# Optimization experiments

Hardware: AMD Instinct MI355X
Metric: run time of the kernel (lower is better)

## Reference

```python
import jax, jax.numpy as jnp
import numpy as np
import math

Z_DIM = 1024
DOWN = 512
UP = 1024
HEADS = 16
ROPE_HD = 64
HEAD_DIM = Z_DIM // HEADS  # 64, used only in softmax scale
V_HD = UP // HEADS


def _rope(x, num_heads, head_dim, base=10000.0):
    # x: [bs, L, num_heads*head_dim] -> [bs, num_heads, L, head_dim]
    bs, L, _ = x.shape
    theta = 1.0 / (base ** (jnp.arange(0, head_dim, 2, dtype=jnp.float32) / head_dim))
    pe = jnp.arange(L, dtype=jnp.float32)[:, None] * theta[None, :]  # [L, hd/2]
    # NOTE: faithful to source, which stores sin(pos) in cos_pos and cos(pos) in sin_pos
    cos_pos = jnp.repeat(jnp.sin(pe), 2, axis=-1)  # [L, hd]
    sin_pos = jnp.repeat(jnp.cos(pe), 2, axis=-1)
    q = x.reshape(bs, L, num_heads, head_dim).transpose(0, 2, 1, 3)
    q2 = jnp.stack([-q[..., 1::2], q[..., ::2]], axis=-1).reshape(q.shape)
    return q * cos_pos + q2 * sin_pos


def setup_inputs() -> dict:
    key = jax.random.key(0)
    ks = jax.random.split(key, 20)
    B, S = 2, 2048
    s = lambda fan_in: 1.0 / math.sqrt(fan_in)
    d = {
        'query': jax.random.normal(ks[0], (B, S, Z_DIM), jnp.float32),
        'key': jax.random.normal(ks[1], (B, S, Z_DIM), jnp.float32),
        'value': jax.random.normal(ks[2], (B, S, Z_DIM), jnp.float32),
        'w_dkv': jax.random.uniform(ks[3], (Z_DIM, DOWN), jnp.float32, -s(Z_DIM), s(Z_DIM)),
        'b_dkv': jnp.zeros((DOWN,), jnp.float32),
        'w_uk': jax.random.uniform(ks[4], (DOWN, UP), jnp.float32, -s(DOWN), s(DOWN)),
        'b_uk': jnp.zeros((UP,), jnp.float32),
        'w_uv': jax.random.uniform(ks[5], (DOWN, UP), jnp.float32, -s(DOWN), s(DOWN)),
        'b_uv': jnp.zeros((UP,), jnp.float32),
        'w_dq': jax.random.uniform(ks[6], (Z_DIM, DOWN), jnp.float32, -s(Z_DIM), s(Z_DIM)),
        'b_dq': jnp.zeros((DOWN,), jnp.float32),
        'w_uq': jax.random.uniform(ks[7], (DOWN, UP), jnp.float32, -s(DOWN), s(DOWN)),
        'b_uq': jnp.zeros((UP,), jnp.float32),
        'w_qr': jax.random.uniform(ks[8], (DOWN, ROPE_HD * HEADS), jnp.float32, -s(DOWN), s(DOWN)),
        'b_qr': jnp.zeros((ROPE_HD * HEADS,), jnp.float32),
        'w_kr': jax.random.uniform(ks[9], (Z_DIM, ROPE_HD), jnp.float32, -s(Z_DIM), s(Z_DIM)),
        'b_kr': jnp.zeros((ROPE_HD,), jnp.float32),
        'w_fc': jax.random.uniform(ks[10], (HEADS * V_HD, Z_DIM), jnp.float32, -s(HEADS * V_HD), s(HEADS * V_HD)),
        'b_fc': jnp.zeros((Z_DIM,), jnp.float32),
    }
    return d


def reference(query, key, value, w_dkv, b_dkv, w_uk, b_uk, w_uv, b_uv,
              w_dq, b_dq, w_uq, b_uq, w_qr, b_qr, w_kr, b_kr, w_fc, b_fc):
    bs, S, _ = query.shape
    c_t_kv = key @ w_dkv + b_dkv                      # [B,S,down]
    k_t_c = c_t_kv @ w_uk + b_uk                      # [B,S,up]
    v_t_c = c_t_kv @ w_uv + b_uv                      # [B,S,up]
    c_t_q = query @ w_dq + b_dq                       # [B,S,down]
    q_t_c = c_t_q @ w_uq + b_uq                       # [B,S,up]
    q_t_r = _rope(c_t_q @ w_qr + b_qr, HEADS, ROPE_HD)  # [B,H,S,rope_hd]
    k_t_r = _rope(key @ w_kr + b_kr, 1, ROPE_HD)         # [B,1,S,rope_hd]

    q_t_c = q_t_c.reshape(bs, S, HEADS, V_HD).transpose(0, 2, 1, 3)  # [B,H,S,dc]
    q = jnp.concatenate([q_t_c, q_t_r], axis=-1)                      # [B,H,S,dc+dr]
    k_t_c = k_t_c.reshape(bs, S, HEADS, V_HD).transpose(0, 2, 1, 3)
    k = jnp.concatenate([k_t_c, jnp.broadcast_to(k_t_r, (bs, HEADS, S, ROPE_HD))], axis=-1)

    scores = jnp.einsum('bhqd,bhkd->bhqk', q, k)
    scale = math.sqrt(HEAD_DIM) + math.sqrt(ROPE_HD)
    attn = jax.nn.softmax(scores / scale, axis=-1)    # dropout is identity (eval / p=0)

    v = v_t_c.reshape(bs, S, HEADS, V_HD).transpose(0, 2, 1, 3)
    out = jnp.einsum('bhqk,bhkd->bhqd', attn, v)      # [B,H,S,v_hd]
    out = out.transpose(0, 2, 1, 3).reshape(bs, S, HEADS * V_HD)
    return out @ w_fc + b_fc
```

## Files before the change

### kernel.cpp

```cpp
#include <hip/hip_runtime.h>
#include <hip/hip_bf16.h>
#include <hip/hip_fp16.h>

typedef __attribute__((ext_vector_type(8))) short    bf16x8;
typedef __attribute__((ext_vector_type(4))) float    f32x4;
typedef __attribute__((ext_vector_type(4))) _Float16 f16x4;
typedef __attribute__((ext_vector_type(2))) __fp16   fp16x2_raw;

typedef const void __attribute__((address_space(1))) gvoid_t;
typedef void __attribute__((address_space(3)))       lvoid_t;

static __device__ __forceinline__ void gload_lds16(const void* g, void* l) {
    __builtin_amdgcn_global_load_lds((gvoid_t*)g, (lvoid_t*)l, 16, 0, 0);
}

static __device__ __forceinline__ short bfbits(float f) {
    union { __hip_bfloat16 h; short s; } u;
    u.h = __float2bfloat16(f);
    return u.s;
}

__global__ __launch_bounds__(256) void cvt_bf16_dual(const float* __restrict__ q,
                                                     const float* __restrict__ k,
                                                     __hip_bfloat16* __restrict__ qd,
                                                     __hip_bfloat16* __restrict__ kd, int n8) {
    int t = blockIdx.x * 256 + threadIdx.x;
    const float* src;
    __hip_bfloat16* dst;
    int i;
    if (t < n8)          { src = q; dst = qd; i = t; }
    else if (t < 2 * n8) { src = k; dst = kd; i = t - n8; }
    else return;
    float4 a = ((const float4*)src)[2 * i];
    float4 b = ((const float4*)src)[2 * i + 1];
    bf16x8 o;
    o[0] = bfbits(a.x); o[1] = bfbits(a.y); o[2] = bfbits(a.z); o[3] = bfbits(a.w);
    o[4] = bfbits(b.x); o[5] = bfbits(b.y); o[6] = bfbits(b.z); o[7] = bfbits(b.w);
    ((bf16x8*)dst)[i] = o;
}

struct TJob { const float* src; __hip_bfloat16* dst; int K, N, tx; };
struct TJobPack { TJob j[8]; int start[8]; };

__global__ __launch_bounds__(256) void transpose_cvt_batch(TJobPack P) {
    __shared__ __hip_bfloat16 tile[64][72];
    const int bid = blockIdx.x;
    int ji = 0;
#pragma unroll
    for (int k = 1; k < 8; ++k) if (bid >= P.start[k]) ji = k;
    const TJob J = P.j[ji];
    const int local = bid - P.start[ji];
    const int kb = (local % J.tx) * 64;
    const int nb = (local / J.tx) * 64;
    const int c  = threadIdx.x & 63;
    const int r0 = threadIdx.x >> 6;
    if (nb < J.N) {
#pragma unroll
        for (int i = 0; i < 16; ++i) {
            int r = r0 + i * 4;
            tile[r][c] = __float2bfloat16(J.src[(size_t)(kb + r) * J.N + nb + c]);
        }
        __syncthreads();
#pragma unroll
        for (int i = 0; i < 16; ++i) {
            int r = r0 + i * 4;
            J.dst[(size_t)(nb + r) * J.K + kb + c] = tile[c][r];
        }
    } else {
        __hip_bfloat16 z = __float2bfloat16(0.0f);
#pragma unroll
        for (int i = 0; i < 16; ++i) {
            int r = r0 + i * 4;
            J.dst[(size_t)(nb + r) * J.K + kb + c] = z;
        }
    }
}

__global__ __launch_bounds__(256) void bias_prep(const float* __restrict__ b_dkv, const float* __restrict__ b_kr,
                                                 const float* __restrict__ b_uk,  const float* __restrict__ b_uv,
                                                 const float* __restrict__ b_uq,  const float* __restrict__ b_qr,
                                                 float* __restrict__ bcat1, float* __restrict__ bcat2,
                                                 float* __restrict__ bcat3) {
    int t = blockIdx.x * 256 + threadIdx.x;
    if (t < 640) {
        bcat1[t] = (t < 512) ? b_dkv[t] : ((t - 512) < 64 ? b_kr[t - 512] : 0.0f);
    } else if (t < 2688) {
        int u = t - 640;
        bcat2[u] = (u < 1024) ? b_uq[u] : b_qr[u - 1024];
    } else if (t < 4736) {
        int u = t - 2688;
        bcat3[u] = (u < 1024) ? b_uk[u] : b_uv[u - 1024];
    }
}

struct GJob {
    const __hip_bfloat16* A; const __hip_bfloat16* Bt; const float* bias;
    void* C0; void* C1; int N, K, lda, ldb, ldc; float scale; int mode;
};

__global__ __launch_bounds__(256) void gemm_dual(GJob j0, GJob j1, int split) {
    __shared__ __align__(16) __hip_bfloat16 sA[2][64 * 32];
    __shared__ __align__(16) __hip_bfloat16 sB[2][128 * 32];
    const GJob J  = (blockIdx.x < (unsigned)split) ? j0 : j1;
    const int bx  = (blockIdx.x < (unsigned)split) ? blockIdx.x : blockIdx.x - split;
    const int tid  = threadIdx.x;
    const int wid  = tid >> 6;
    const int lane = tid & 63;
    const int lr   = lane & 15;
    const int lg   = lane >> 4;
    const int mb   = blockIdx.y * 64;
    const int nb   = bx * 128;
    const int wr   = (wid >> 1) * 32;
    const int wc   = (wid & 1) * 64;

    auto stage = [&](int bufi, int k0) {
        {
            int e   = wid * 512 + lane * 8;
            int row = e >> 5, col = e & 31;
            gload_lds16(J.A + (size_t)(mb + row) * J.lda + (k0 + col), &sA[bufi][wid * 512]);
        }
#pragma unroll
        for (int j = 0; j < 2; ++j) {
            int cb  = wid * 2 + j;
            int e   = cb * 512 + lane * 8;
            int row = e >> 5, col = e & 31;
            gload_lds16(J.Bt + (size_t)(nb + row) * J.ldb + (k0 + col), &sB[bufi][cb * 512]);
        }
    };

    f32x4 acc[2][4] = {};
    const int nt = J.K / 32;
    stage(0, 0);
    asm volatile("s_waitcnt vmcnt(0)" ::: "memory");
    __syncthreads();

    for (int t = 0; t < nt; ++t) {
        const int cur = t & 1;
        if (t + 1 < nt) stage(cur ^ 1, (t + 1) * 32);
        bf16x8 af[2], bfr[4];
#pragma unroll
        for (int m = 0; m < 2; ++m)
            af[m] = *(const bf16x8*)&sA[cur][(wr + m * 16 + lr) * 32 + lg * 8];
#pragma unroll
        for (int n = 0; n < 4; ++n)
            bfr[n] = *(const bf16x8*)&sB[cur][(wc + n * 16 + lr) * 32 + lg * 8];
#pragma unroll
        for (int m = 0; m < 2; ++m)
#pragma unroll
            for (int n = 0; n < 4; ++n)
                acc[m][n] = __builtin_amdgcn_mfma_f32_16x16x32_bf16(af[m], bfr[n], acc[m][n], 0, 0, 0);
        asm volatile("s_waitcnt vmcnt(0)" ::: "memory");
        __syncthreads();
    }

#pragma unroll
    for (int n = 0; n < 4; ++n) {
        int col  = nb + wc + n * 16 + lr;
        float bv = J.bias ? J.bias[col] : 0.0f;
#pragma unroll
        for (int m = 0; m < 2; ++m) {
#pragma unroll
            for (int r = 0; r < 4; ++r) {
                int row    = mb + wr + m * 16 + lg * 4 + r;
                float val  = (acc[m][n][r] + bv) * J.scale;
                if (J.mode == 1) {
                    ((float*)J.C0)[(size_t)row * J.ldc + col] = val;
                } else if (J.mode == 3) {
                    if (col < 1024) ((__hip_bfloat16*)J.C0)[(size_t)row * 1024 + col] = __float2bfloat16(val);
                    else            ((_Float16*)J.C1)[(size_t)row * 1024 + col - 1024] = (_Float16)val;
                } else {
                    ((__hip_bfloat16*)J.C0)[(size_t)row * J.ldc + col] = __float2bfloat16(val);
                }
            }
        }
    }
}

__global__ __launch_bounds__(256) void misc_kernel(const _Float16* __restrict__ vtc,
                                                   _Float16* __restrict__ vtcT,
                                                   __hip_bfloat16* __restrict__ qrope,
                                                   __hip_bfloat16* __restrict__ krope,
                                                   int R, int S) {
    __shared__ _Float16 tile[64][72];
    const int tp  = R >> 2;
    const int bid = blockIdx.x;
    if (bid < tp) {
        const int cb = (bid % 16) * 64;
        const int rb = (bid / 16) * 64;
        const int c4 = (threadIdx.x & 15) * 4;
        const int rl = threadIdx.x >> 4;
#pragma unroll
        for (int i = 0; i < 4; ++i) {
            int row = rl + i * 16;
            *(f16x4*)&tile[row][c4] = *(const f16x4*)&vtc[(size_t)(rb + row) * 1024 + cb + c4];
        }
        __syncthreads();
#pragma unroll
        for (int i = 0; i < 4; ++i) {
            int orow = rl + i * 16;
            f16x4 v;
#pragma unroll
            for (int j = 0; j < 4; ++j) v[j] = tile[c4 + j][orow];
            *(f16x4*)&vtcT[(size_t)(cb + orow) * R + rb + c4] = v;
        }
        return;
    }
    int t = (bid - tp) * 256 + threadIdx.x;
    const int nq = R * 512;
    __hip_bfloat16* x;
    int i, row, rowstride, hh;
    if (t < nq)               { i = t & 31; hh = (t >> 5) & 15; row = t >> 9; x = qrope; rowstride = 2048; }
    else if (t < nq + R * 32) { t -= nq; i = t & 31; hh = 0; row = t >> 5; x = krope; rowstride = 640; }
    else return;
    int pos = row % S;
    float theta = __expf(-0.28782313662425572f * (float)i);
    float pe = (float)pos * theta;
    float sp, cp;
    sincosf(pe, &sp, &cp);
    size_t idx = (size_t)row * rowstride + hh * 64 + 2 * i;
    float x0 = __bfloat162float(x[idx]);
    float x1 = __bfloat162float(x[idx + 1]);
    x[idx]     = __float2bfloat16(x0 * sp - x1 * cp);
    x[idx + 1] = __float2bfloat16(x1 * sp + x0 * cp);
}

__global__ __launch_bounds__(256, 2) void attn_kernel(const __hip_bfloat16* __restrict__ qcat,
                                                      const __hip_bfloat16* __restrict__ ktc,
                                                      const __hip_bfloat16* __restrict__ kr,
                                                      const _Float16* __restrict__ vtcT,
                                                      __hip_bfloat16* __restrict__ outp,
                                                      int S, int R) {
    __shared__ __align__(16) char lds[2][24 * 1024];
    const int tid  = threadIdx.x;
    const int wid  = tid >> 6;
    const int lane = tid & 63;
    const int lr   = lane & 15;
    const int lg   = lane >> 4;

    const int NQ   = S / 128;
    const int L    = blockIdx.x;
    const int slot = L >> 3;
    const int gg   = (L & 7) + 8 * (slot / NQ);
    const int qt   = slot % NQ;
    const int h    = gg & 15;
    const int b    = gg >> 4;
    const size_t base = (size_t)b * S;
    const int qb   = qt * 128 + wid * 32;

    auto stage = [&](int bufi, int kt) {
        char* bufK = lds[bufi];
        char* bufV = lds[bufi] + 16 * 1024;
#pragma unroll
        for (int j = 0; j < 4; ++j) {
            int c   = wid * 4 + j;
            int rho = c * 4 + (lane >> 4);
            int u   = (lane & 15) ^ (rho & 15);
            const __hip_bfloat16* src = (u < 8)
                ? ktc + (base + kt + rho) * 1024 + h * 64 + u * 8
                : kr  + (base + kt + rho) * 640 + (u & 7) * 8;
            gload_lds16(src, bufK + c * 1024);
        }
#pragma unroll
        for (int j = 0; j < 2; ++j) {
            int c   = wid * 2 + j;
            int rho = c * 8 + (lane >> 3);
            int u   = (lane & 7) ^ (rho & 7);
            gload_lds16(vtcT + (size_t)(h * 64 + rho) * R + base + kt + u * 8,
                        bufV + c * 1024);
        }
    };

    bf16x8 qf[2][4];
#pragma unroll
    for (int g = 0; g < 2; ++g) {
        size_t row = base + qb + g * 16 + lr;
        const __hip_bfloat16* pq = qcat + row * 2048 + h * 64;
        qf[g][0] = *(const bf16x8*)(pq + lg * 8);
        qf[g][1] = *(const bf16x8*)(pq + 32 + lg * 8);
        qf[g][2] = *(const bf16x8*)(pq + 1024 + lg * 8);
        qf[g][3] = *(const bf16x8*)(pq + 1024 + 32 + lg * 8);
    }

    f32x4 oacc[2][4] = {};
    float lrun[2] = {0.0f, 0.0f};

    const int NT = S / 64;
    stage(0, 0);
    __syncthreads();

    for (int t = 0; t < NT; ++t) {
        const int cur = t & 1;
        if (t + 1 < NT) stage(cur ^ 1, (t + 1) * 64);

        const char* bufK = lds[cur];
        const char* bufV = lds[cur] + 16 * 1024;

        f32x4 sacc[2][4] = {};
#pragma unroll
        for (int st = 0; st < 4; ++st) {
            bf16x8 kf[4];
#pragma unroll
            for (int c = 0; c < 4; ++c)
                kf[c] = *(const bf16x8*)(bufK + (st * 16 + lr) * 256 +
                                         (((c * 4 + lg) ^ lr) << 4));
#pragma unroll
            for (int g = 0; g < 2; ++g)
#pragma unroll
                for (int c = 0; c < 4; ++c)
                    sacc[g][st] = __builtin_amdgcn_mfma_f32_16x16x32_bf16(kf[c], qf[g][c], sacc[g][st], 0, 0, 0);
        }

        f16x4 vf[4][4];
#pragma unroll
        for (int st = 0; st < 4; ++st)
#pragma unroll
            for (int vt = 0; vt < 4; ++vt)
                vf[st][vt] = *(const f16x4*)(bufV + (vt * 16 + lr) * 128 +
                                             (((st * 2 + (lg >> 1)) ^ (lr & 7)) << 4) + (lg & 1) * 8);

#pragma unroll
        for (int g = 0; g < 2; ++g) {
            float p[4][4];
#pragma unroll
            for (int st = 0; st < 4; ++st)
#pragma unroll
                for (int r = 0; r < 4; ++r) {
                    p[st][r] = __builtin_exp2f(sacc[g][st][r]);
                    lrun[g] += p[st][r];
                }
#pragma unroll
            for (int st = 0; st < 4; ++st) {
                union { fp16x2_raw h2[2]; f16x4 v; } pu;
                pu.h2[0] = __builtin_amdgcn_cvt_pkrtz(p[st][0], p[st][1]);
                pu.h2[1] = __builtin_amdgcn_cvt_pkrtz(p[st][2], p[st][3]);
#pragma unroll
                for (int vt = 0; vt < 4; ++vt)
                    oacc[g][vt] = __builtin_amdgcn_mfma_f32_16x16x16f16(vf[st][vt], pu.v, oacc[g][vt], 0, 0, 0);
            }
        }
        __syncthreads();
    }

#pragma unroll
    for (int g = 0; g < 2; ++g) {
        lrun[g] += __shfl_xor(lrun[g], 16);
        lrun[g] += __shfl_xor(lrun[g], 32);
        float inv = 1.0f / lrun[g];
        size_t rowoff = (base + qb + g * 16 + lr) << 10;
#pragma unroll
        for (int vt = 0; vt < 4; ++vt)
#pragma unroll
            for (int r = 0; r < 4; ++r)
                outp[rowoff + h * 64 + vt * 16 + lg * 4 + r] =
                    __float2bfloat16(oacc[g][vt][r] * inv);
    }
}

extern "C" void kernel_launch(void* const* d_in, const int* in_sizes, int n_in,
                              void* d_out, int out_size, void* d_ws, size_t ws_size,
                              hipStream_t stream) {
    const float* query = (const float*)d_in[0];
    const float* key   = (const float*)d_in[1];
    const float* w_dkv = (const float*)d_in[3];
    const float* b_dkv = (const float*)d_in[4];
    const float* w_uk  = (const float*)d_in[5];
    const float* b_uk  = (const float*)d_in[6];
    const float* w_uv  = (const float*)d_in[7];
    const float* b_uv  = (const float*)d_in[8];
    const float* w_dq  = (const float*)d_in[9];
    const float* b_dq  = (const float*)d_in[10];
    const float* w_uq  = (const float*)d_in[11];
    const float* b_uq  = (const float*)d_in[12];
    const float* w_qr  = (const float*)d_in[13];
    const float* b_qr  = (const float*)d_in[14];
    const float* w_kr  = (const float*)d_in[15];
    const float* b_kr  = (const float*)d_in[16];
    const float* w_fc  = (const float*)d_in[17];
    const float* b_fc  = (const float*)d_in[18];

    const int B = 2;
    const int R = in_sizes[0] / 1024;
    const int S = R / B;
    const float QSCALE = 1.4426950408889634f / 16.0f;

    char* ws = (char*)d_ws;
    size_t off = 0;
    auto alloc = [&](size_t bytes) -> char* {
        char* p = ws + off;
        off += (bytes + 255) & ~(size_t)255;
        return p;
    };

    __hip_bfloat16* q_bf  = (__hip_bfloat16*)alloc((size_t)R * 1024 * 2);
    __hip_bfloat16* k_bf  = (__hip_bfloat16*)alloc((size_t)R * 1024 * 2);
    __hip_bfloat16* wcat1 = (__hip_bfloat16*)alloc(640 * 1024 * 2);
    __hip_bfloat16* wdq_t = (__hip_bfloat16*)alloc(512 * 1024 * 2);
    __hip_bfloat16* wcat3 = (__hip_bfloat16*)alloc(2048 * 512 * 2);
    __hip_bfloat16* wcat2 = (__hip_bfloat16*)alloc(2048 * 512 * 2);
    __hip_bfloat16* wfc_t = (__hip_bfloat16*)alloc(1024 * 1024 * 2);
    float*          bcat1 = (float*)alloc(640 * 4);
    float*          bcat2 = (float*)alloc(2048 * 4);
    float*          bcat3 = (float*)alloc(2048 * 4);
    __hip_bfloat16* ckkr  = (__hip_bfloat16*)alloc((size_t)R * 640 * 2);
    __hip_bfloat16* c_q   = (__hip_bfloat16*)alloc((size_t)R * 512 * 2);
    __hip_bfloat16* ktc   = (__hip_bfloat16*)alloc((size_t)R * 1024 * 2);
    _Float16*       vtc   = (_Float16*)alloc((size_t)R * 1024 * 2);
    _Float16*       vtcT  = (_Float16*)alloc((size_t)R * 1024 * 2);
    __hip_bfloat16* qcat  = (__hip_bfloat16*)alloc((size_t)R * 2048 * 2);
    __hip_bfloat16* attn_out = q_bf;

    cvt_bf16_dual<<<dim3(2 * R * 1024 / 8 / 256), 256, 0, stream>>>(query, key, q_bf, k_bf, R * 1024 / 8);

    TJobPack P;
    P.j[0] = {w_dkv, wcat1,              1024, 512,  16};
    P.j[1] = {w_kr,  wcat1 + 512 * 1024, 1024, 64,   16};
    P.j[2] = {w_dq,  wdq_t,              1024, 512,  16};
    P.j[3] = {w_uk,  wcat3,              512,  1024, 8};
    P.j[4] = {w_uv,  wcat3 + 1024 * 512, 512,  1024, 8};
    P.j[5] = {w_uq,  wcat2,              512,  1024, 8};
    P.j[6] = {w_qr,  wcat2 + 1024 * 512, 512,  1024, 8};
    P.j[7] = {w_fc,  wfc_t,              1024, 1024, 16};
    int st = 0;
    const int counts[8] = {128, 32, 128, 128, 128, 128, 128, 256};
    for (int i = 0; i < 8; ++i) { P.start[i] = st; st += counts[i]; }
    transpose_cvt_batch<<<dim3(st), 256, 0, stream>>>(P);

    bias_prep<<<dim3(19), 256, 0, stream>>>(b_dkv, b_kr, b_uk, b_uv, b_uq, b_qr, bcat1, bcat2, bcat3);

    GJob ja0 = {k_bf, wcat1, bcat1, ckkr, nullptr, 640, 1024, 1024, 1024, 640, 1.0f, 0};
    GJob ja1 = {q_bf, wdq_t, b_dq,  c_q,  nullptr, 512, 1024, 1024, 1024, 512, 1.0f, 0};
    gemm_dual<<<dim3(9, R / 64), 256, 0, stream>>>(ja0, ja1, 5);

    GJob jb0 = {ckkr, wcat3, bcat3, ktc,  vtc,     2048, 512, 640, 512, 1024, 1.0f,   3};
    GJob jb1 = {c_q,  wcat2, bcat2, qcat, nullptr, 2048, 512, 512, 512, 2048, QSCALE, 0};
    gemm_dual<<<dim3(32, R / 64), 256, 0, stream>>>(jb0, jb1, 16);

    {
        int tp = R >> 2;
        int ropeBlocks = (R * 512 + R * 32 + 255) / 256;
        misc_kernel<<<dim3(tp + ropeBlocks), 256, 0, stream>>>(vtc, vtcT, qcat + 1024, ckkr + 512, R, S);
    }

    attn_kernel<<<dim3((S / 128) * 16 * B), 256, 0, stream>>>(qcat, ktc, ckkr + 512, vtcT, attn_out, S, R);

    GJob jc0 = {attn_out, wfc_t, b_fc, d_out, nullptr, 1024, 1024, 1024, 1024, 1024, 1.0f, 1};
    gemm_dual<<<dim3(8, R / 64), 256, 0, stream>>>(jc0, jc0, 8);
}
```

Measured before the change: 188.6 us.

## Split attention over two key chunks with a merge kernel; fuse input bf16 conversion into GEMM

The attention kernel now splits the key range into two halves, doubling the grid. It uses single-buffered LDS with occupancy 4 and writes unnormalized fp16 partial outputs plus row sums. A new merge kernel adds the two partials, normalizes and produces the bf16 input for the output projection. Separately, the fp32-to-bf16 cast of query and key is folded into the first GEMM's A-tile load through registers, removing the standalone conversion kernel and its buffers. The trade-off is an extra partial-output write and read, one more launch, and lost global-to-LDS async loads for the first GEMM.

```diff
diff --git a/kernel.cpp b/kernel.cpp
--- a/kernel.cpp
+++ b/kernel.cpp
@@ -5,6 +5,7 @@
 typedef __attribute__((ext_vector_type(8))) short    bf16x8;
 typedef __attribute__((ext_vector_type(4))) float    f32x4;
 typedef __attribute__((ext_vector_type(4))) _Float16 f16x4;
+typedef __attribute__((ext_vector_type(8))) _Float16 f16x8;
 typedef __attribute__((ext_vector_type(2))) __fp16   fp16x2_raw;
 
 typedef const void __attribute__((address_space(1))) gvoid_t;
@@ -18,25 +19,6 @@
     union { __hip_bfloat16 h; short s; } u;
     u.h = __float2bfloat16(f);
     return u.s;
-}
-
-__global__ __launch_bounds__(256) void cvt_bf16_dual(const float* __restrict__ q,
-                                                     const float* __restrict__ k,
-                                                     __hip_bfloat16* __restrict__ qd,
-                                                     __hip_bfloat16* __restrict__ kd, int n8) {
-    int t = blockIdx.x * 256 + threadIdx.x;
-    const float* src;
-    __hip_bfloat16* dst;
-    int i;
-    if (t < n8)          { src = q; dst = qd; i = t; }
-    else if (t < 2 * n8) { src = k; dst = kd; i = t - n8; }
-    else return;
-    float4 a = ((const float4*)src)[2 * i];
-    float4 b = ((const float4*)src)[2 * i + 1];
-    bf16x8 o;
-    o[0] = bfbits(a.x); o[1] = bfbits(a.y); o[2] = bfbits(a.z); o[3] = bfbits(a.w);
-    o[4] = bfbits(b.x); o[5] = bfbits(b.y); o[6] = bfbits(b.z); o[7] = bfbits(b.w);
-    ((bf16x8*)dst)[i] = o;
 }
 
 struct TJob { const float* src; __hip_bfloat16* dst; int K, N, tx; };
@@ -94,8 +76,8 @@
 }
 
 struct GJob {
-    const __hip_bfloat16* A; const __hip_bfloat16* Bt; const float* bias;
-    void* C0; void* C1; int N, K, lda, ldb, ldc; float scale; int mode;
+    const void* A; const __hip_bfloat16* Bt; const float* bias;
+    void* C0; void* C1; int N, K, lda, ldb, ldc; float scale; int mode; int afp32;
 };
 
 __global__ __launch_bounds__(256) void gemm_dual(GJob j0, GJob j1, int split) {
@@ -112,13 +94,27 @@
     const int nb   = bx * 128;
     const int wr   = (wid >> 1) * 32;
     const int wc   = (wid & 1) * 64;
-
-    auto stage = [&](int bufi, int k0) {
-        {
-            int e   = wid * 512 + lane * 8;
-            int row = e >> 5, col = e & 31;
-            gload_lds16(J.A + (size_t)(mb + row) * J.lda + (k0 + col), &sA[bufi][wid * 512]);
-        }
+    const int ar   = (wid * 512 + lane * 8) >> 5;
+    const int ac   = (wid * 512 + lane * 8) & 31;
+
+    float4 a0, a1;
+
+    auto loadA_f32 = [&](int k0) {
+        const float* s = (const float*)J.A + (size_t)(mb + ar) * J.lda + (k0 + ac);
+        a0 = ((const float4*)s)[0];
+        a1 = ((const float4*)s)[1];
+    };
+    auto writeA = [&](int bufi) {
+        bf16x8 o;
+        o[0] = bfbits(a0.x); o[1] = bfbits(a0.y); o[2] = bfbits(a0.z); o[3] = bfbits(a0.w);
+        o[4] = bfbits(a1.x); o[5] = bfbits(a1.y); o[6] = bfbits(a1.z); o[7] = bfbits(a1.w);
+        *(bf16x8*)&sA[bufi][wid * 512 + lane * 8] = o;
+    };
+    auto stageA_lds = [&](int bufi, int k0) {
+        gload_lds16((const __hip_bfloat16*)J.A + (size_t)(mb + ar) * J.lda + (k0 + ac),
+                    &sA[bufi][wid * 512]);
+    };
+    auto stageB = [&](int bufi, int k0) {
 #pragma unroll
         for (int j = 0; j < 2; ++j) {
             int cb  = wid * 2 + j;
@@ -130,13 +126,17 @@
 
     f32x4 acc[2][4] = {};
     const int nt = J.K / 32;
-    stage(0, 0);
-    asm volatile("s_waitcnt vmcnt(0)" ::: "memory");
+    if (J.afp32) { loadA_f32(0); stageB(0, 0); asm volatile("s_waitcnt vmcnt(0)" ::: "memory"); writeA(0); }
+    else         { stageA_lds(0, 0); stageB(0, 0); asm volatile("s_waitcnt vmcnt(0)" ::: "memory"); }
     __syncthreads();
 
     for (int t = 0; t < nt; ++t) {
         const int cur = t & 1;
-        if (t + 1 < nt) stage(cur ^ 1, (t + 1) * 32);
+        if (t + 1 < nt) {
+            if (J.afp32) loadA_f32((t + 1) * 32);
+            else         stageA_lds(cur ^ 1, (t + 1) * 32);
+            stageB(cur ^ 1, (t + 1) * 32);
+        }
         bf16x8 af[2], bfr[4];
 #pragma unroll
         for (int m = 0; m < 2; ++m)
@@ -150,6 +150,7 @@
             for (int n = 0; n < 4; ++n)
                 acc[m][n] = __builtin_amdgcn_mfma_f32_16x16x32_bf16(af[m], bfr[n], acc[m][n], 0, 0, 0);
         asm volatile("s_waitcnt vmcnt(0)" ::: "memory");
+        if (J.afp32 && t + 1 < nt) writeA(cur ^ 1);
         __syncthreads();
     }
 
@@ -224,32 +225,37 @@
     x[idx + 1] = __float2bfloat16(x1 * sp + x0 * cp);
 }
 
-__global__ __launch_bounds__(256, 2) void attn_kernel(const __hip_bfloat16* __restrict__ qcat,
+__global__ __launch_bounds__(256, 4) void attn_kernel(const __hip_bfloat16* __restrict__ qcat,
                                                       const __hip_bfloat16* __restrict__ ktc,
                                                       const __hip_bfloat16* __restrict__ kr,
                                                       const _Float16* __restrict__ vtcT,
-                                                      __hip_bfloat16* __restrict__ outp,
+                                                      _Float16* __restrict__ po,
+                                                      float* __restrict__ pl,
                                                       int S, int R) {
-    __shared__ __align__(16) char lds[2][24 * 1024];
+    __shared__ __align__(16) char lds[24 * 1024];
     const int tid  = threadIdx.x;
     const int wid  = tid >> 6;
     const int lane = tid & 63;
     const int lr   = lane & 15;
     const int lg   = lane >> 4;
 
-    const int NQ   = S / 128;
-    const int L    = blockIdx.x;
-    const int slot = L >> 3;
-    const int gg   = (L & 7) + 8 * (slot / NQ);
-    const int qt   = slot % NQ;
-    const int h    = gg & 15;
-    const int b    = gg >> 4;
+    const int NQ    = S / 128;
+    const int L     = blockIdx.x;
+    const int slot  = L >> 3;
+    const int sub   = slot % (NQ * 2);
+    const int gg    = (L & 7) + 8 * (slot / (NQ * 2));
+    const int qt    = sub >> 1;
+    const int chunk = sub & 1;
+    const int h     = gg & 15;
+    const int b     = gg >> 4;
+    const int S2    = S >> 1;
+    const int c0    = chunk * S2;
     const size_t base = (size_t)b * S;
-    const int qb   = qt * 128 + wid * 32;
-
-    auto stage = [&](int bufi, int kt) {
-        char* bufK = lds[bufi];
-        char* bufV = lds[bufi] + 16 * 1024;
+    const int qb    = qt * 128 + wid * 32;
+
+    auto stage = [&](int kt) {
+        char* bufK = lds;
+        char* bufV = lds + 16 * 1024;
 #pragma unroll
         for (int j = 0; j < 4; ++j) {
             int c   = wid * 4 + j;
@@ -284,16 +290,13 @@
     f32x4 oacc[2][4] = {};
     float lrun[2] = {0.0f, 0.0f};
 
-    const int NT = S / 64;
-    stage(0, 0);
+    stage(c0);
+    asm volatile("s_waitcnt vmcnt(0)" ::: "memory");
     __syncthreads();
 
-    for (int t = 0; t < NT; ++t) {
-        const int cur = t & 1;
-        if (t + 1 < NT) stage(cur ^ 1, (t + 1) * 64);
-
-        const char* bufK = lds[cur];
-        const char* bufV = lds[cur] + 16 * 1024;
+    for (int kt = c0; kt < c0 + S2; kt += 64) {
+        const char* bufK = lds;
+        const char* bufV = lds + 16 * 1024;
 
         f32x4 sacc[2][4] = {};
 #pragma unroll
@@ -317,6 +320,9 @@
             for (int vt = 0; vt < 4; ++vt)
                 vf[st][vt] = *(const f16x4*)(bufV + (vt * 16 + lr) * 128 +
                                              (((st * 2 + (lg >> 1)) ^ (lr & 7)) << 4) + (lg & 1) * 8);
+
+        __syncthreads();
+        if (kt + 64 < c0 + S2) stage(kt + 64);
 
 #pragma unroll
         for (int g = 0; g < 2; ++g) {
@@ -338,6 +344,7 @@
                     oacc[g][vt] = __builtin_amdgcn_mfma_f32_16x16x16f16(vf[st][vt], pu.v, oacc[g][vt], 0, 0, 0);
             }
         }
+        asm volatile("s_waitcnt vmcnt(0)" ::: "memory");
         __syncthreads();
     }
 
@@ -345,15 +352,36 @@
     for (int g = 0; g < 2; ++g) {
         lrun[g] += __shfl_xor(lrun[g], 16);
         lrun[g] += __shfl_xor(lrun[g], 32);
-        float inv = 1.0f / lrun[g];
-        size_t rowoff = (base + qb + g * 16 + lr) << 10;
-#pragma unroll
-        for (int vt = 0; vt < 4; ++vt)
-#pragma unroll
-            for (int r = 0; r < 4; ++r)
-                outp[rowoff + h * 64 + vt * 16 + lg * 4 + r] =
-                    __float2bfloat16(oacc[g][vt][r] * inv);
-    }
+        size_t row = base + qb + g * 16 + lr;
+        size_t rowoff = ((size_t)chunk * R + row) << 10;
+#pragma unroll
+        for (int vt = 0; vt < 4; ++vt) {
+            union { fp16x2_raw h2[2]; f16x4 v; } pu;
+            pu.h2[0] = __builtin_amdgcn_cvt_pkrtz(oacc[g][vt][0], oacc[g][vt][1]);
+            pu.h2[1] = __builtin_amdgcn_cvt_pkrtz(oacc[g][vt][2], oacc[g][vt][3]);
+            *(f16x4*)&po[rowoff + h * 64 + vt * 16 + lg * 4] = pu.v;
+        }
+        if (lg == 0) pl[((size_t)chunk * R + row) * 16 + h] = lrun[g];
+    }
+}
+
+__global__ __launch_bounds__(256) void merge_attn(const _Float16* __restrict__ po,
+                                                  const float* __restrict__ pl,
+                                                  __hip_bfloat16* __restrict__ out, int R) {
+    int t = blockIdx.x * 256 + threadIdx.x;
+    size_t t8 = (size_t)t * 8;
+    int row = (int)(t8 >> 10);
+    int c   = (int)(t8 & 1023);
+    int h   = c >> 6;
+    float l = pl[(size_t)row * 16 + h] + pl[((size_t)R + row) * 16 + h];
+    float inv = 1.0f / l;
+    f16x8 a = *(const f16x8*)&po[t8];
+    f16x8 b = *(const f16x8*)&po[(size_t)R * 1024 + t8];
+    bf16x8 o;
+#pragma unroll
+    for (int j = 0; j < 8; ++j)
+        o[j] = bfbits(((float)a[j] + (float)b[j]) * inv);
+    *(bf16x8*)&out[t8] = o;
 }
 
 extern "C" void kernel_launch(void* const* d_in, const int* in_sizes, int n_in,
@@ -391,8 +419,6 @@
         return p;
     };
 
-    __hip_bfloat16* q_bf  = (__hip_bfloat16*)alloc((size_t)R * 1024 * 2);
-    __hip_bfloat16* k_bf  = (__hip_bfloat16*)alloc((size_t)R * 1024 * 2);
     __hip_bfloat16* wcat1 = (__hip_bfloat16*)alloc(640 * 1024 * 2);
     __hip_bfloat16* wdq_t = (__hip_bfloat16*)alloc(512 * 1024 * 2);
     __hip_bfloat16* wcat3 = (__hip_bfloat16*)alloc(2048 * 512 * 2);
@@ -407,9 +433,9 @@
     _Float16*       vtc   = (_Float16*)alloc((size_t)R * 1024 * 2);
     _Float16*       vtcT  = (_Float16*)alloc((size_t)R * 1024 * 2);
     __hip_bfloat16* qcat  = (__hip_bfloat16*)alloc((size_t)R * 2048 * 2);
-    __hip_bfloat16* attn_out = q_bf;
-
-    cvt_bf16_dual<<<dim3(2 * R * 1024 / 8 / 256), 256, 0, stream>>>(query, key, q_bf, k_bf, R * 1024 / 8);
+    _Float16*       po    = (_Float16*)alloc((size_t)2 * R * 1024 * 2);
+    float*          pl    = (float*)c_q;
+    __hip_bfloat16* attn_out = (__hip_bfloat16*)vtc;
 
     TJobPack P;
     P.j[0] = {w_dkv, wcat1,              1024, 512,  16};
@@ -427,12 +453,12 @@
 
     bias_prep<<<dim3(19), 256, 0, stream>>>(b_dkv, b_kr, b_uk, b_uv, b_uq, b_qr, bcat1, bcat2, bcat3);
 
-    GJob ja0 = {k_bf, wcat1, bcat1, ckkr, nullptr, 640, 1024, 1024, 1024, 640, 1.0f, 0};
-    GJob ja1 = {q_bf, wdq_t, b_dq,  c_q,  nullptr, 512, 1024, 1024, 1024, 512, 1.0f, 0};
+    GJob ja0 = {key,   wcat1, bcat1, ckkr, nullptr, 640, 1024, 1024, 1024, 640, 1.0f, 0, 1};
+    GJob ja1 = {query, wdq_t, b_dq,  c_q,  nullptr, 512, 1024, 1024, 1024, 512, 1.0f, 0, 1};
     gemm_dual<<<dim3(9, R / 64), 256, 0, stream>>>(ja0, ja1, 5);
 
-    GJob jb0 = {ckkr, wcat3, bcat3, ktc,  vtc,     2048, 512, 640, 512, 1024, 1.0f,   3};
-    GJob jb1 = {c_q,  wcat2, bcat2, qcat, nullptr, 2048, 512, 512, 512, 2048, QSCALE, 0};
+    GJob jb0 = {ckkr, wcat3, bcat3, ktc,  vtc,     2048, 512, 640, 512, 1024, 1.0f,   3, 0};
+    GJob jb1 = {c_q,  wcat2, bcat2, qcat, nullptr, 2048, 512, 512, 512, 2048, QSCALE, 0, 0};
     gemm_dual<<<dim3(32, R / 64), 256, 0, stream>>>(jb0, jb1, 16);
 
     {
@@ -441,8 +467,9 @@
         misc_kernel<<<dim3(tp + ropeBlocks), 256, 0, stream>>>(vtc, vtcT, qcat + 1024, ckkr + 512, R, S);
     }
 
-    attn_kernel<<<dim3((S / 128) * 16 * B), 256, 0, stream>>>(qcat, ktc, ckkr + 512, vtcT, attn_out, S, R);
-
-    GJob jc0 = {attn_out, wfc_t, b_fc, d_out, nullptr, 1024, 1024, 1024, 1024, 1024, 1.0f, 1};
+    attn_kernel<<<dim3((S / 128) * 2 * 16 * B), 256, 0, stream>>>(qcat, ktc, ckkr + 512, vtcT, po, pl, S, R);
+    merge_attn<<<dim3(R * 1024 / 8 / 256), 256, 0, stream>>>(po, pl, attn_out, R);
+
+    GJob jc0 = {attn_out, wfc_t, b_fc, d_out, nullptr, 1024, 1024, 1024, 1024, 1024, 1.0f, 1, 0};
     gemm_dual<<<dim3(8, R / 64), 256, 0, stream>>>(jc0, jc0, 8);
 }
```

Result: slower. 314.5 us (+66.7%).
